# Kernel optimization log

Hardware: AMD Instinct MI355X
Metric: run time of the kernel (lower is better)

Reference implementation:

```python
import jax, jax.numpy as jnp
import numpy as np

B, N, D_IN, D, H, DEPTH = 8, 1024, 256, 256, 8, 3
HD = D // H
EPS = 1e-5


def setup_inputs() -> dict:
    key = jax.random.key(0)
    ks = jax.random.split(key, 16)
    x = jax.random.normal(ks[0], (B, N, D_IN), dtype=jnp.float32)
    # binary adjacency with self-loops (requires_grad=False Parameter in torch)
    adj = (jax.random.uniform(ks[1], (N, N)) < 0.03).astype(jnp.float32)
    adj = jnp.maximum(adj, jnp.eye(N, dtype=jnp.float32))
    s = 1.0 / np.sqrt(D)
    W0 = jax.random.uniform(ks[2], (D, D_IN), minval=-s, maxval=s)
    Wq = jax.random.uniform(ks[3], (DEPTH, D, D), minval=-s, maxval=s)
    Wk = jax.random.uniform(ks[4], (DEPTH, D, D), minval=-s, maxval=s)
    Wv = jax.random.uniform(ks[5], (DEPTH, D, D), minval=-s, maxval=s)
    Wo = jax.random.uniform(ks[6], (DEPTH, D, D), minval=-s, maxval=s)
    bq = jnp.zeros((DEPTH, D)); bk = jnp.zeros((DEPTH, D))
    bv = jnp.zeros((DEPTH, D)); bo = jnp.zeros((DEPTH, D))
    gamma = jnp.ones((DEPTH, D)); beta = jnp.zeros((DEPTH, D))
    return {"x": x, "adj": adj, "W0": W0, "Wq": Wq, "bq": bq, "Wk": Wk,
            "bk": bk, "Wv": Wv, "bv": bv, "Wo": Wo, "bo": bo,
            "gamma": gamma, "beta": beta}


def _layernorm(h, g, b):
    mu = jnp.mean(h, axis=-1, keepdims=True)
    var = jnp.mean(jnp.square(h - mu), axis=-1, keepdims=True)
    return (h - mu) * jax.lax.rsqrt(var + EPS) * g + b


def reference(x, adj, W0, Wq, bq, Wk, bk, Wv, bv, Wo, bo, gamma, beta):
    # input projection (no bias)
    h = jnp.einsum('bnd,ed->bne', x, W0)  # [B,N,D]
    mask = adj[None, None] > 0            # [1,1,N,N]
    scale = 1.0 / jnp.sqrt(jnp.float32(HD))
    atten = None
    for i in range(DEPTH):
        q = (jnp.einsum('bnd,ed->bne', h, Wq[i]) + bq[i]).reshape(B, N, H, HD)
        k = (jnp.einsum('bnd,ed->bne', h, Wk[i]) + bk[i]).reshape(B, N, H, HD)
        v = (jnp.einsum('bnd,ed->bne', h, Wv[i]) + bv[i]).reshape(B, N, H, HD)
        scores = jnp.einsum('bihd,bjhd->bhij', q, k) * scale  # [B,H,N,N]
        scores = jnp.where(mask, scores, -1e9)
        a = jax.nn.softmax(scores, axis=-1)
        o = jnp.einsum('bhij,bjhd->bihd', a, v).reshape(B, N, D)
        y = jnp.einsum('bnd,ed->bne', o, Wo[i]) + bo[i]
        h = _layernorm(h + y, gamma[i], beta[i])
        a_mean = jnp.mean(a, axis=1)  # head-averaged [B,N,N]
        atten = a_mean if atten is None else jnp.einsum('bij,bjk->bik', a_mean, atten)
    return h, atten
```

## Files before the change

### kernel.cpp

```cpp
#include <hip/hip_runtime.h>

typedef unsigned short u16;
typedef unsigned int   u32;
typedef float  f32x4  __attribute__((ext_vector_type(4)));
typedef __bf16 bf16x8 __attribute__((ext_vector_type(8)));
typedef u32    u32x4  __attribute__((ext_vector_type(4)));
typedef u32    u32x2  __attribute__((ext_vector_type(2)));

#define Bb  8
#define Nn  1024
#define Dd  256
#define Hh  8
#define HDd 32
#define CAP 96

__device__ __forceinline__ float bf2f(u16 s){
  u32 u = ((u32)s) << 16; float f; __builtin_memcpy(&f, &u, 4); return f;
}
__device__ __forceinline__ u16 f2bf(float f){
  u32 u; __builtin_memcpy(&u, &f, 4);
  u = (u + 0x7fffu + ((u >> 16) & 1u)) >> 16;
  return (u16)u;
}
__device__ __forceinline__ f32x4 mfma16(bf16x8 a, bf16x8 b, f32x4 c){
  return __builtin_amdgcn_mfma_f32_16x16x32_bf16(a, b, c, 0, 0, 0);
}
__device__ __forceinline__ bf16x8 ld_bf8(const u16* p){
  u32x4 u = *(const u32x4*)p; bf16x8 r; __builtin_memcpy(&r, &u, 16); return r;
}

__global__ void f32_to_bf16(const float* __restrict__ src, u16* __restrict__ dst, int n){
  int i = (blockIdx.x * 256 + threadIdx.x) * 4;
  if (i < n){
    f32x4 v = *(const f32x4*)(src + i);
    u32x2 p;
    p[0] = (u32)f2bf(v[0]) | ((u32)f2bf(v[1]) << 16);
    p[1] = (u32)f2bf(v[2]) | ((u32)f2bf(v[3]) << 16);
    *(u32x2*)(dst + i) = p;
  }
}

__global__ void conv_w4(const float* __restrict__ wq, const float* __restrict__ wk,
                        const float* __restrict__ wv, const float* __restrict__ wo,
                        u16* __restrict__ dst){
  int g = blockIdx.x * 256 + threadIdx.x;
  int sec = g / 49152, off = (g - sec * 49152) * 4;
  const float* src = (sec == 0 ? wq : sec == 1 ? wk : sec == 2 ? wv : wo);
  f32x4 v = *(const f32x4*)(src + off);
  u32x2 p;
  p[0] = (u32)f2bf(v[0]) | ((u32)f2bf(v[1]) << 16);
  p[1] = (u32)f2bf(v[2]) | ((u32)f2bf(v[3]) << 16);
  *(u32x2*)(dst + sec * 196608 + off) = p;
}

__global__ void bias_concat(const float* __restrict__ bq, const float* __restrict__ bk,
                            const float* __restrict__ bv, float* __restrict__ bqkv){
  int t = threadIdx.x;
  for (int l = 0; l < 3; ++l){
    bqkv[l*768 +       t] = bq[l*256 + t];
    bqkv[l*768 + 256 + t] = bk[l*256 + t];
    bqkv[l*768 + 512 + t] = bv[l*256 + t];
  }
}

__global__ void adj_to_bits(const float* __restrict__ adj, u32* __restrict__ bits){
  int w = blockIdx.x * 256 + threadIdx.x;
  const float* p = adj + (long)w * 32;
  u32 m = 0;
  #pragma unroll
  for (int t = 0; t < 32; t += 4){
    f32x4 v = *(const f32x4*)(p + t);
    if (v[0] != 0.f) m |= 1u << (t+0);
    if (v[1] != 0.f) m |= 1u << (t+1);
    if (v[2] != 0.f) m |= 1u << (t+2);
    if (v[3] != 0.f) m |= 1u << (t+3);
  }
  bits[w] = m;
}

__global__ __launch_bounds__(256) void nbr_build(const u32* __restrict__ bits,
                                                 u16* __restrict__ idx, int* __restrict__ cnt){
  int i = blockIdx.x * 256 + threadIdx.x;
  int c = 0;
  for (int w = 0; w < 32; ++w){
    u32 wd = bits[i*32 + w];
    while (wd){
      int bi = __ffs(wd) - 1; wd &= wd - 1;
      if (c < CAP) idx[(long)i*CAP + c] = (u16)(w*32 + bi);
      ++c;
    }
  }
  cnt[i] = (c < CAP) ? c : CAP;
}

template<bool HBC, bool HBR, bool OF, bool OB>
__global__ __launch_bounds__(256,2) void gemm_bt(
    const u16* __restrict__ A, int lda, long sA,
    const u16* __restrict__ Bt, int ldb, long sB,
    float* __restrict__ Cf, u16* __restrict__ Cb, int ldc, long sC,
    int K, const float* __restrict__ bc, long sbc, const float* __restrict__ br)
{
  __shared__ u16 As[128][40];
  __shared__ u16 Bs[128][40];
  const int bz = blockIdx.z;
  const u16* Ap = A + (long)bz * sA;
  const u16* Bp = Bt + (long)bz * sB;
  const long co = (long)bz * sC;
  const int m0 = blockIdx.y * 128, n0 = blockIdx.x * 128;
  const int tid = threadIdx.x, wave = tid >> 6, lane = tid & 63;
  const int arow = lane & 15, agrp = lane >> 4;
  const int wr = (wave >> 1) * 64, wc = (wave & 1) * 64;
  const int srow = tid >> 1, sch = (tid & 1) * 16;
  const u16* ga = Ap + (long)(m0 + srow) * lda + sch;
  const u16* gb = Bp + (long)(n0 + srow) * ldb + sch;
  f32x4 acc[4][4] = {};
  for (int kb = 0; kb < K; kb += 32){
    u32x4 a0 = *(const u32x4*)ga; u32x4 a1 = *(const u32x4*)(ga + 8);
    u32x4 b0 = *(const u32x4*)gb; u32x4 b1 = *(const u32x4*)(gb + 8);
    __syncthreads();
    *(u32x4*)&As[srow][sch] = a0; *(u32x4*)&As[srow][sch + 8] = a1;
    *(u32x4*)&Bs[srow][sch] = b0; *(u32x4*)&Bs[srow][sch + 8] = b1;
    __syncthreads();
    ga += 32; gb += 32;
    bf16x8 af[4], bv[4];
    #pragma unroll
    for (int f = 0; f < 4; ++f){
      af[f] = ld_bf8(&As[wr + f*16 + arow][agrp*8]);
      bv[f] = ld_bf8(&Bs[wc + f*16 + arow][agrp*8]);
    }
    #pragma unroll
    for (int fm = 0; fm < 4; ++fm)
      #pragma unroll
      for (int fn = 0; fn < 4; ++fn)
        acc[fm][fn] = mfma16(af[fm], bv[fn], acc[fm][fn]);
  }
  #pragma unroll
  for (int fm = 0; fm < 4; ++fm){
    #pragma unroll
    for (int fn = 0; fn < 4; ++fn){
      int j = n0 + wc + fn*16 + arow;
      float badd = 0.f;
      if (HBC) badd = bc[(long)bz*sbc + j];
      #pragma unroll
      for (int r = 0; r < 4; ++r){
        int i = m0 + wr + fm*16 + agrp*4 + r;
        float v = acc[fm][fn][r] + badd;
        if (HBR) v += br[i];
        long idx = co + (long)i * ldc + j;
        if (OF) Cf[idx] = v;
        if (OB) Cb[idx] = f2bf(v);
      }
    }
  }
}

__global__ __launch_bounds__(256) void attn_sparse(
    const u16* __restrict__ qkv,
    u16* __restrict__ ob,
    const u16* __restrict__ idxg, const int* __restrict__ cntg,
    float* __restrict__ amv)
{
  __shared__ float qs[4][256];
  __shared__ float E[4][CAP][8];
  __shared__ float invl[4][8];
  __shared__ u16   idxl[4][CAP];
  __shared__ int   cntl[4];
  const int b = blockIdx.y, i0 = blockIdx.x * 4;
  const int tid = threadIdx.x, w = tid >> 6, lane = tid & 63;
  const float SCALE = 0.17677669529663687f;

  { int e = tid * 4, rr = e >> 8, c = e & 255;
    u32x2 uv = *(const u32x2*)(qkv + ((long)(b*Nn + i0 + rr)) * 768 + c);
    qs[rr][c+0] = SCALE * bf2f((u16)(uv[0] & 0xffff));
    qs[rr][c+1] = SCALE * bf2f((u16)(uv[0] >> 16));
    qs[rr][c+2] = SCALE * bf2f((u16)(uv[1] & 0xffff));
    qs[rr][c+3] = SCALE * bf2f((u16)(uv[1] >> 16)); }
  for (int s = tid; s < 4*CAP; s += 256){
    int rr = s / CAP, ss = s - rr*CAP;
    idxl[rr][ss] = idxg[(long)(i0 + rr)*CAP + ss];
  }
  if (tid < 4) cntl[tid] = cntg[i0 + tid];
  __syncthreads();

  const int i = i0 + w;
  const int cnt = cntl[w];

  { const f32x4 qreg = *(const f32x4*)&qs[w][lane*4];
    const int h = lane >> 3;
    int s = 0;
    for (; s + 2 <= cnt; s += 2){
      int ja = idxl[w][s], jb = idxl[w][s+1];
      u32x2 ka = *(const u32x2*)(qkv + ((long)(b*Nn + ja))*768 + 256 + lane*4);
      u32x2 kb = *(const u32x2*)(qkv + ((long)(b*Nn + jb))*768 + 256 + lane*4);
      float pa = qreg[0]*bf2f((u16)(ka[0]&0xffff)) + qreg[1]*bf2f((u16)(ka[0]>>16))
               + qreg[2]*bf2f((u16)(ka[1]&0xffff)) + qreg[3]*bf2f((u16)(ka[1]>>16));
      float pb = qreg[0]*bf2f((u16)(kb[0]&0xffff)) + qreg[1]*bf2f((u16)(kb[0]>>16))
               + qreg[2]*bf2f((u16)(kb[1]&0xffff)) + qreg[3]*bf2f((u16)(kb[1]>>16));
      pa += __shfl_xor(pa, 1, 64); pa += __shfl_xor(pa, 2, 64); pa += __shfl_xor(pa, 4, 64);
      pb += __shfl_xor(pb, 1, 64); pb += __shfl_xor(pb, 2, 64); pb += __shfl_xor(pb, 4, 64);
      if ((lane & 7) == 0){ E[w][s][h] = pa; E[w][s+1][h] = pb; }
    }
    if (s < cnt){
      int ja = idxl[w][s];
      u32x2 ka = *(const u32x2*)(qkv + ((long)(b*Nn + ja))*768 + 256 + lane*4);
      float pa = qreg[0]*bf2f((u16)(ka[0]&0xffff)) + qreg[1]*bf2f((u16)(ka[0]>>16))
               + qreg[2]*bf2f((u16)(ka[1]&0xffff)) + qreg[3]*bf2f((u16)(ka[1]>>16));
      pa += __shfl_xor(pa, 1, 64); pa += __shfl_xor(pa, 2, 64); pa += __shfl_xor(pa, 4, 64);
      if ((lane & 7) == 0) E[w][s][h] = pa;
    }
  }
  __syncthreads();

  { const int h = lane >> 3, k = lane & 7;
    float m = -3.0e38f;
    for (int s = k; s < cnt; s += 8) m = fmaxf(m, E[w][s][h]);
    m = fmaxf(m, __shfl_xor(m, 1, 64));
    m = fmaxf(m, __shfl_xor(m, 2, 64));
    m = fmaxf(m, __shfl_xor(m, 4, 64));
    float l = 0.f;
    for (int s = k; s < cnt; s += 8){
      float e = __expf(E[w][s][h] - m);
      E[w][s][h] = e; l += e;
    }
    l += __shfl_xor(l, 1, 64);
    l += __shfl_xor(l, 2, 64);
    l += __shfl_xor(l, 4, 64);
    if (k == 0) invl[w][h] = 1.f / l;
  }
  __syncthreads();

  { f32x4 i0v = *(f32x4*)&invl[w][0], i1v = *(f32x4*)&invl[w][4];
    for (int s = lane; s < cnt; s += 64){
      f32x4 e0 = *(f32x4*)&E[w][s][0], e1 = *(f32x4*)&E[w][s][4];
      float a = e0[0]*i0v[0] + e0[1]*i0v[1] + e0[2]*i0v[2] + e0[3]*i0v[3]
              + e1[0]*i1v[0] + e1[1]*i1v[1] + e1[2]*i1v[2] + e1[3]*i1v[3];
      amv[((long)(b*Nn + i))*CAP + s] = a * 0.125f;
    }
  }

  { const int d0 = lane * 4, h = lane >> 3;
    f32x4 acc = {0.f, 0.f, 0.f, 0.f};
    int s = 0;
    for (; s + 2 <= cnt; s += 2){
      int ja = idxl[w][s], jb = idxl[w][s+1];
      u32x2 va = *(const u32x2*)(qkv + ((long)(b*Nn + ja)) * 768 + 512 + d0);
      u32x2 vb = *(const u32x2*)(qkv + ((long)(b*Nn + jb)) * 768 + 512 + d0);
      float ea = E[w][s][h], eb = E[w][s+1][h];
      acc[0] += ea * bf2f((u16)(va[0] & 0xffff)) + eb * bf2f((u16)(vb[0] & 0xffff));
      acc[1] += ea * bf2f((u16)(va[0] >> 16))    + eb * bf2f((u16)(vb[0] >> 16));
      acc[2] += ea * bf2f((u16)(va[1] & 0xffff)) + eb * bf2f((u16)(vb[1] & 0xffff));
      acc[3] += ea * bf2f((u16)(va[1] >> 16))    + eb * bf2f((u16)(vb[1] >> 16));
    }
    if (s < cnt){
      int ja = idxl[w][s];
      u32x2 va = *(const u32x2*)(qkv + ((long)(b*Nn + ja)) * 768 + 512 + d0);
      float ea = E[w][s][h];
      acc[0] += ea * bf2f((u16)(va[0] & 0xffff));
      acc[1] += ea * bf2f((u16)(va[0] >> 16));
      acc[2] += ea * bf2f((u16)(va[1] & 0xffff));
      acc[3] += ea * bf2f((u16)(va[1] >> 16));
    }
    float nl = invl[w][h];
    u32x2 pb;
    pb[0] = (u32)f2bf(acc[0]*nl) | ((u32)f2bf(acc[1]*nl) << 16);
    pb[1] = (u32)f2bf(acc[2]*nl) | ((u32)f2bf(acc[3]*nl) << 16);
    *(u32x2*)(ob + ((long)(b*Nn + i)) * 256 + d0) = pb;
  }
}

__global__ __launch_bounds__(256) void sp_gemm1(
    const float* __restrict__ amv1, const float* __restrict__ amv0,
    const u16* __restrict__ idxg, const int* __restrict__ cntg,
    u16* __restrict__ P1)
{
  __shared__ float accum[1024];
  __shared__ u16 idxl[CAP];
  __shared__ u16 cjl[CAP];
  __shared__ float v1[CAP];
  const int b = blockIdx.y, i = blockIdx.x, tid = threadIdx.x;
  { f32x4 z = {0.f,0.f,0.f,0.f}; *(f32x4*)&accum[tid*4] = z; }
  const int cnt = cntg[i];
  if (tid < CAP){
    idxl[tid] = idxg[(long)i*CAP + tid];
    v1[tid]   = amv1[((long)(b*Nn + i))*CAP + tid];
  }
  __syncthreads();
  if (tid < CAP)
    cjl[tid] = (tid < cnt) ? (u16)cntg[idxl[tid]] : (u16)0;
  __syncthreads();
  const int npairs = cnt * 64;
  for (int p = tid; p < npairs; p += 512){
    const int sa = p >> 6, ta = p & 63;
    const int ja = idxl[sa], ca = cjl[sa];
    const float va = v1[sa];
    int colA = 0, colA2 = 0; float prA = 0.f, prA2 = 0.f;
    const bool dA  = ta < ca;
    const bool dA2 = ta + 64 < ca;
    if (dA){  colA  = idxg[(long)ja*CAP + ta];
              prA   = va * amv0[((long)(b*Nn + ja))*CAP + ta]; }
    if (dA2){ colA2 = idxg[(long)ja*CAP + ta + 64];
              prA2  = va * amv0[((long)(b*Nn + ja))*CAP + ta + 64]; }
    const int pb = p + 256;
    const bool hasB = pb < npairs;
    const int sb = pb >> 6, tb = pb & 63;
    int jb = 0, cb = 0; float vb = 0.f;
    if (hasB){ jb = idxl[sb]; cb = cjl[sb]; vb = v1[sb]; }
    int colB = 0, colB2 = 0; float prB = 0.f, prB2 = 0.f;
    const bool dB  = hasB && tb < cb;
    const bool dB2 = hasB && tb + 64 < cb;
    if (dB){  colB  = idxg[(long)jb*CAP + tb];
              prB   = vb * amv0[((long)(b*Nn + jb))*CAP + tb]; }
    if (dB2){ colB2 = idxg[(long)jb*CAP + tb + 64];
              prB2  = vb * amv0[((long)(b*Nn + jb))*CAP + tb + 64]; }
    if (dA)  atomicAdd(&accum[colA],  prA);
    if (dA2) atomicAdd(&accum[colA2], prA2);
    if (dB)  atomicAdd(&accum[colB],  prB);
    if (dB2) atomicAdd(&accum[colB2], prB2);
  }
  __syncthreads();
  int c0 = tid * 4;
  u32x2 pb;
  pb[0] = (u32)f2bf(accum[c0])   | ((u32)f2bf(accum[c0+1]) << 16);
  pb[1] = (u32)f2bf(accum[c0+2]) | ((u32)f2bf(accum[c0+3]) << 16);
  *(u32x2*)(P1 + ((long)(b*Nn + i))*1024 + c0) = pb;
}

__global__ __launch_bounds__(256) void sp_gemm2(
    const float* __restrict__ amv2, const u16* __restrict__ P1,
    const u16* __restrict__ idxg, const int* __restrict__ cntg,
    float* __restrict__ out)
{
  __shared__ u16 idxl[CAP];
  __shared__ float v2[CAP];
  const int b = blockIdx.y, i = blockIdx.x, tid = threadIdx.x;
  const int cnt = cntg[i];
  if (tid < CAP){
    idxl[tid] = idxg[(long)i*CAP + tid];
    v2[tid]   = amv2[((long)(b*Nn + i))*CAP + tid];
  }
  __syncthreads();
  f32x4 acc = {0.f, 0.f, 0.f, 0.f};
  const int c0 = tid * 4;
  int s = 0;
  for (; s + 2 <= cnt; s += 2){
    int ja = idxl[s], jb = idxl[s+1];
    float ea = v2[s], eb = v2[s+1];
    u32x2 va = *(const u32x2*)(P1 + ((long)(b*Nn + ja))*1024 + c0);
    u32x2 vb = *(const u32x2*)(P1 + ((long)(b*Nn + jb))*1024 + c0);
    acc[0] += ea * bf2f((u16)(va[0] & 0xffff)) + eb * bf2f((u16)(vb[0] & 0xffff));
    acc[1] += ea * bf2f((u16)(va[0] >> 16))    + eb * bf2f((u16)(vb[0] >> 16));
    acc[2] += ea * bf2f((u16)(va[1] & 0xffff)) + eb * bf2f((u16)(vb[1] & 0xffff));
    acc[3] += ea * bf2f((u16)(va[1] >> 16))    + eb * bf2f((u16)(vb[1] >> 16));
  }
  if (s < cnt){
    int ja = idxl[s];
    float ea = v2[s];
    u32x2 va = *(const u32x2*)(P1 + ((long)(b*Nn + ja))*1024 + c0);
    acc[0] += ea * bf2f((u16)(va[0] & 0xffff));
    acc[1] += ea * bf2f((u16)(va[0] >> 16));
    acc[2] += ea * bf2f((u16)(va[1] & 0xffff));
    acc[3] += ea * bf2f((u16)(va[1] >> 16));
  }
  *(f32x4*)(out + ((long)(b*Nn + i))*1024 + c0) = acc;
}

__global__ __launch_bounds__(256) void ln_kernel(
    const float* __restrict__ hin, const float* __restrict__ y,
    float* __restrict__ hout, u16* __restrict__ hb, float* __restrict__ outf,
    const float* __restrict__ g, const float* __restrict__ be)
{
  int row  = blockIdx.x * 4 + (threadIdx.x >> 6);
  int lane = threadIdx.x & 63;
  f32x4 v = *(const f32x4*)(hin + (long)row*Dd + lane*4)
          + *(const f32x4*)(y   + (long)row*Dd + lane*4);
  float s = v[0] + v[1] + v[2] + v[3];
  #pragma unroll
  for (int off = 32; off; off >>= 1) s += __shfl_xor(s, off, 64);
  float mu = s * (1.f/256.f);
  f32x4 d = v - mu;
  float q2 = d[0]*d[0] + d[1]*d[1] + d[2]*d[2] + d[3]*d[3];
  #pragma unroll
  for (int off = 32; off; off >>= 1) q2 += __shfl_xor(q2, off, 64);
  float rs = rsqrtf(q2 * (1.f/256.f) + 1e-5f);
  f32x4 ov;
  #pragma unroll
  for (int p = 0; p < 4; ++p)
    ov[p] = d[p] * rs * g[lane*4 + p] + be[lane*4 + p];
  *(f32x4*)(hout + (long)row*Dd + lane*4) = ov;
  if (hb){
    u32x2 pb;
    pb[0] = (u32)f2bf(ov[0]) | ((u32)f2bf(ov[1]) << 16);
    pb[1] = (u32)f2bf(ov[2]) | ((u32)f2bf(ov[3]) << 16);
    *(u32x2*)(hb + (long)row*Dd + lane*4) = pb;
  }
  if (outf)
    *(f32x4*)(outf + (long)row*Dd + lane*4) = ov;
}

extern "C" void kernel_launch(void* const* d_in, const int* in_sizes, int n_in,
                              void* d_out, int out_size, void* d_ws, size_t ws_size,
                              hipStream_t stream)
{
  (void)in_sizes; (void)n_in; (void)out_size; (void)ws_size;
  const float* x   = (const float*)d_in[0];
  const float* adj = (const float*)d_in[1];
  const float* W0  = (const float*)d_in[2];
  const float* Wq  = (const float*)d_in[3];
  const float* bq  = (const float*)d_in[4];
  const float* Wk  = (const float*)d_in[5];
  const float* bk  = (const float*)d_in[6];
  const float* Wv  = (const float*)d_in[7];
  const float* bv  = (const float*)d_in[8];
  const float* Wo  = (const float*)d_in[9];
  const float* bo  = (const float*)d_in[10];
  const float* gm  = (const float*)d_in[11];
  const float* bt  = (const float*)d_in[12];
  float* outf  = (float*)d_out;
  float* outat = outf + (long)Bb * Nn * Dd;

  char* w = (char*)d_ws;
  u16* W0b  = (u16*)w; w += 131072;
  u16* Wqb  = (u16*)w; w += 393216;
  u16* Wkb  = (u16*)w; w += 393216;
  u16* Wvb  = (u16*)w; w += 393216;
  u16* Wob  = (u16*)w; w += 393216;
  float* bqkv = (float*)w; w += 9216;
  u32* bitsg = (u32*)w; w += 131072;
  u16* idxg  = (u16*)w; w += 1024*CAP*2;
  int* cntg  = (int*)w; w += 4096;
  u16* xb  = (u16*)w; w += 4194304;
  u16* hb  = (u16*)w; w += 4194304;
  u16* qkv = (u16*)w; w += (long)Bb*Nn*768*2;
  u16* ob  = (u16*)w; w += 4194304;
  float* hbuf = (float*)w; w += 8388608;
  float* ybuf = (float*)w; w += 8388608;
  float* amv0 = (float*)w; w += (long)Bb*Nn*CAP*4;
  float* amv1 = (float*)w; w += (long)Bb*Nn*CAP*4;
  float* amv2 = (float*)w; w += (long)Bb*Nn*CAP*4;
  u16* P1   = (u16*)w; w += 16777216;
  float* amvl[3] = {amv0, amv1, amv2};

  dim3 blk(256);
  f32_to_bf16<<<2048, blk, 0, stream>>>(x,  xb,  2097152);
  f32_to_bf16<<<64,   blk, 0, stream>>>(W0, W0b, 65536);
  conv_w4<<<768, blk, 0, stream>>>(Wq, Wk, Wv, Wo, Wqb);
  bias_concat<<<1, blk, 0, stream>>>(bq, bk, bv, bqkv);
  adj_to_bits<<<128, blk, 0, stream>>>(adj, bitsg);
  nbr_build<<<4, blk, 0, stream>>>(bitsg, idxg, cntg);

  gemm_bt<false,false,true,true><<<dim3(2,64,1), blk, 0, stream>>>(
      xb, 256, 0, W0b, 256, 0, hbuf, hb, 256, 0, 256, nullptr, 0, nullptr);

  for (int l = 0; l < 3; ++l){
    gemm_bt<true,false,false,true><<<dim3(2,64,3), blk, 0, stream>>>(
        hb, 256, 0, Wqb + (long)l*65536, 256, 196608,
        nullptr, qkv, 768, 256, 256, bqkv + l*768, 256, nullptr);
    attn_sparse<<<dim3(256,8), blk, 0, stream>>>(qkv, ob, idxg, cntg, amvl[l]);
    gemm_bt<true,false,true,false><<<dim3(2,64,1), blk, 0, stream>>>(
        ob, 256, 0, Wob + (long)l*65536, 256, 0, ybuf, nullptr, 256, 0, 256,
        bo + l*256, 0, nullptr);
    ln_kernel<<<dim3(2048), blk, 0, stream>>>(
        hbuf, ybuf, hbuf, (l < 2 ? hb : nullptr), (l < 2 ? nullptr : outf),
        gm + l*256, bt + l*256);
    if (l == 1)
      sp_gemm1<<<dim3(1024,8), blk, 0, stream>>>(amv1, amv0, idxg, cntg, P1);
    if (l == 2)
      sp_gemm2<<<dim3(1024,8), blk, 0, stream>>>(amv2, P1, idxg, cntg, outat);
  }
}
```

Before: 305.7 us.

## Write layer-0 attention densely and reuse row-gather kernel for both attention products

Layer 0 attention weights are now scattered as bf16 into a dense zeroed NxN buffer, so the first attention product becomes a sparse-row gather over dense rows instead of a shared-memory atomic scatter. The two product kernels merge into one templated kernel. Weight and bias conversion kernels are fused into one launch. The trade is a 16 MB memset plus dense bf16 reads, and extra rounding of the layer-0 weights to bf16.

New measurement: 287.1 us. -6.1%, faster.

```diff
diff --git a/kernel.cpp b/kernel.cpp
--- a/kernel.cpp
+++ b/kernel.cpp
@@ -40,27 +40,34 @@
   }
 }
 
-__global__ void conv_w4(const float* __restrict__ wq, const float* __restrict__ wk,
-                        const float* __restrict__ wv, const float* __restrict__ wo,
-                        u16* __restrict__ dst){
-  int g = blockIdx.x * 256 + threadIdx.x;
-  int sec = g / 49152, off = (g - sec * 49152) * 4;
-  const float* src = (sec == 0 ? wq : sec == 1 ? wk : sec == 2 ? wv : wo);
+__global__ void conv_w5(const float* __restrict__ w0, const float* __restrict__ wq,
+                        const float* __restrict__ wk, const float* __restrict__ wv,
+                        const float* __restrict__ wo, u16* __restrict__ dst,
+                        const float* __restrict__ bq, const float* __restrict__ bk,
+                        const float* __restrict__ bv, float* __restrict__ bqkv){
+  if (blockIdx.x == 832){
+    int t = threadIdx.x;
+    for (int l = 0; l < 3; ++l){
+      bqkv[l*768 +       t] = bq[l*256 + t];
+      bqkv[l*768 + 256 + t] = bk[l*256 + t];
+      bqkv[l*768 + 512 + t] = bv[l*256 + t];
+    }
+    return;
+  }
+  int g4 = (blockIdx.x * 256 + threadIdx.x) * 4;
+  const float* src;
+  int off;
+  if (g4 < 65536){ src = w0; off = g4; }
+  else {
+    int g = g4 - 65536;
+    int sec = g / 196608; off = g - sec * 196608;
+    src = (sec == 0 ? wq : sec == 1 ? wk : sec == 2 ? wv : wo);
+  }
   f32x4 v = *(const f32x4*)(src + off);
   u32x2 p;
   p[0] = (u32)f2bf(v[0]) | ((u32)f2bf(v[1]) << 16);
   p[1] = (u32)f2bf(v[2]) | ((u32)f2bf(v[3]) << 16);
-  *(u32x2*)(dst + sec * 196608 + off) = p;
-}
-
-__global__ void bias_concat(const float* __restrict__ bq, const float* __restrict__ bk,
-                            const float* __restrict__ bv, float* __restrict__ bqkv){
-  int t = threadIdx.x;
-  for (int l = 0; l < 3; ++l){
-    bqkv[l*768 +       t] = bq[l*256 + t];
-    bqkv[l*768 + 256 + t] = bk[l*256 + t];
-    bqkv[l*768 + 512 + t] = bv[l*256 + t];
-  }
+  *(u32x2*)(dst + g4) = p;
 }
 
 __global__ void adj_to_bits(const float* __restrict__ adj, u32* __restrict__ bits){
@@ -158,7 +165,8 @@
     const u16* __restrict__ qkv,
     u16* __restrict__ ob,
     const u16* __restrict__ idxg, const int* __restrict__ cntg,
-    float* __restrict__ amv)
+    float* __restrict__ amv,
+    u16* __restrict__ amd, int dense)
 {
   __shared__ float qs[4][256];
   __shared__ float E[4][CAP][8];
@@ -234,7 +242,9 @@
       f32x4 e0 = *(f32x4*)&E[w][s][0], e1 = *(f32x4*)&E[w][s][4];
       float a = e0[0]*i0v[0] + e0[1]*i0v[1] + e0[2]*i0v[2] + e0[3]*i0v[3]
               + e1[0]*i1v[0] + e1[1]*i1v[1] + e1[2]*i1v[2] + e1[3]*i1v[3];
-      amv[((long)(b*Nn + i))*CAP + s] = a * 0.125f;
+      a *= 0.125f;
+      if (dense) amd[((long)(b*Nn + i))*1024 + idxl[w][s]] = f2bf(a);
+      else       amv[((long)(b*Nn + i))*CAP + s] = a;
     }
   }
 
@@ -268,75 +278,20 @@
   }
 }
 
-__global__ __launch_bounds__(256) void sp_gemm1(
-    const float* __restrict__ amv1, const float* __restrict__ amv0,
+template<bool OUTF32>
+__global__ __launch_bounds__(256) void sp_chain(
+    const float* __restrict__ wts,
+    const u16* __restrict__ rows,
     const u16* __restrict__ idxg, const int* __restrict__ cntg,
-    u16* __restrict__ P1)
-{
-  __shared__ float accum[1024];
-  __shared__ u16 idxl[CAP];
-  __shared__ u16 cjl[CAP];
-  __shared__ float v1[CAP];
-  const int b = blockIdx.y, i = blockIdx.x, tid = threadIdx.x;
-  { f32x4 z = {0.f,0.f,0.f,0.f}; *(f32x4*)&accum[tid*4] = z; }
-  const int cnt = cntg[i];
-  if (tid < CAP){
-    idxl[tid] = idxg[(long)i*CAP + tid];
-    v1[tid]   = amv1[((long)(b*Nn + i))*CAP + tid];
-  }
-  __syncthreads();
-  if (tid < CAP)
-    cjl[tid] = (tid < cnt) ? (u16)cntg[idxl[tid]] : (u16)0;
-  __syncthreads();
-  const int npairs = cnt * 64;
-  for (int p = tid; p < npairs; p += 512){
-    const int sa = p >> 6, ta = p & 63;
-    const int ja = idxl[sa], ca = cjl[sa];
-    const float va = v1[sa];
-    int colA = 0, colA2 = 0; float prA = 0.f, prA2 = 0.f;
-    const bool dA  = ta < ca;
-    const bool dA2 = ta + 64 < ca;
-    if (dA){  colA  = idxg[(long)ja*CAP + ta];
-              prA   = va * amv0[((long)(b*Nn + ja))*CAP + ta]; }
-    if (dA2){ colA2 = idxg[(long)ja*CAP + ta + 64];
-              prA2  = va * amv0[((long)(b*Nn + ja))*CAP + ta + 64]; }
-    const int pb = p + 256;
-    const bool hasB = pb < npairs;
-    const int sb = pb >> 6, tb = pb & 63;
-    int jb = 0, cb = 0; float vb = 0.f;
-    if (hasB){ jb = idxl[sb]; cb = cjl[sb]; vb = v1[sb]; }
-    int colB = 0, colB2 = 0; float prB = 0.f, prB2 = 0.f;
-    const bool dB  = hasB && tb < cb;
-    const bool dB2 = hasB && tb + 64 < cb;
-    if (dB){  colB  = idxg[(long)jb*CAP + tb];
-              prB   = vb * amv0[((long)(b*Nn + jb))*CAP + tb]; }
-    if (dB2){ colB2 = idxg[(long)jb*CAP + tb + 64];
-              prB2  = vb * amv0[((long)(b*Nn + jb))*CAP + tb + 64]; }
-    if (dA)  atomicAdd(&accum[colA],  prA);
-    if (dA2) atomicAdd(&accum[colA2], prA2);
-    if (dB)  atomicAdd(&accum[colB],  prB);
-    if (dB2) atomicAdd(&accum[colB2], prB2);
-  }
-  __syncthreads();
-  int c0 = tid * 4;
-  u32x2 pb;
-  pb[0] = (u32)f2bf(accum[c0])   | ((u32)f2bf(accum[c0+1]) << 16);
-  pb[1] = (u32)f2bf(accum[c0+2]) | ((u32)f2bf(accum[c0+3]) << 16);
-  *(u32x2*)(P1 + ((long)(b*Nn + i))*1024 + c0) = pb;
-}
-
-__global__ __launch_bounds__(256) void sp_gemm2(
-    const float* __restrict__ amv2, const u16* __restrict__ P1,
-    const u16* __restrict__ idxg, const int* __restrict__ cntg,
-    float* __restrict__ out)
+    u16* __restrict__ dstb, float* __restrict__ dstf)
 {
   __shared__ u16 idxl[CAP];
-  __shared__ float v2[CAP];
+  __shared__ float wl[CAP];
   const int b = blockIdx.y, i = blockIdx.x, tid = threadIdx.x;
   const int cnt = cntg[i];
   if (tid < CAP){
     idxl[tid] = idxg[(long)i*CAP + tid];
-    v2[tid]   = amv2[((long)(b*Nn + i))*CAP + tid];
+    wl[tid]   = wts[((long)(b*Nn + i))*CAP + tid];
   }
   __syncthreads();
   f32x4 acc = {0.f, 0.f, 0.f, 0.f};
@@ -344,9 +299,9 @@
   int s = 0;
   for (; s + 2 <= cnt; s += 2){
     int ja = idxl[s], jb = idxl[s+1];
-    float ea = v2[s], eb = v2[s+1];
-    u32x2 va = *(const u32x2*)(P1 + ((long)(b*Nn + ja))*1024 + c0);
-    u32x2 vb = *(const u32x2*)(P1 + ((long)(b*Nn + jb))*1024 + c0);
+    float ea = wl[s], eb = wl[s+1];
+    u32x2 va = *(const u32x2*)(rows + ((long)(b*Nn + ja))*1024 + c0);
+    u32x2 vb = *(const u32x2*)(rows + ((long)(b*Nn + jb))*1024 + c0);
     acc[0] += ea * bf2f((u16)(va[0] & 0xffff)) + eb * bf2f((u16)(vb[0] & 0xffff));
     acc[1] += ea * bf2f((u16)(va[0] >> 16))    + eb * bf2f((u16)(vb[0] >> 16));
     acc[2] += ea * bf2f((u16)(va[1] & 0xffff)) + eb * bf2f((u16)(vb[1] & 0xffff));
@@ -354,14 +309,21 @@
   }
   if (s < cnt){
     int ja = idxl[s];
-    float ea = v2[s];
-    u32x2 va = *(const u32x2*)(P1 + ((long)(b*Nn + ja))*1024 + c0);
+    float ea = wl[s];
+    u32x2 va = *(const u32x2*)(rows + ((long)(b*Nn + ja))*1024 + c0);
     acc[0] += ea * bf2f((u16)(va[0] & 0xffff));
     acc[1] += ea * bf2f((u16)(va[0] >> 16));
     acc[2] += ea * bf2f((u16)(va[1] & 0xffff));
     acc[3] += ea * bf2f((u16)(va[1] >> 16));
   }
-  *(f32x4*)(out + ((long)(b*Nn + i))*1024 + c0) = acc;
+  if (OUTF32){
+    *(f32x4*)(dstf + ((long)(b*Nn + i))*1024 + c0) = acc;
+  } else {
+    u32x2 pb;
+    pb[0] = (u32)f2bf(acc[0]) | ((u32)f2bf(acc[1]) << 16);
+    pb[1] = (u32)f2bf(acc[2]) | ((u32)f2bf(acc[3]) << 16);
+    *(u32x2*)(dstb + ((long)(b*Nn + i))*1024 + c0) = pb;
+  }
 }
 
 __global__ __launch_bounds__(256) void ln_kernel(
@@ -420,10 +382,7 @@
 
   char* w = (char*)d_ws;
   u16* W0b  = (u16*)w; w += 131072;
-  u16* Wqb  = (u16*)w; w += 393216;
-  u16* Wkb  = (u16*)w; w += 393216;
-  u16* Wvb  = (u16*)w; w += 393216;
-  u16* Wob  = (u16*)w; w += 393216;
+  u16* Wqb  = (u16*)w; w += 4*393216;
   float* bqkv = (float*)w; w += 9216;
   u32* bitsg = (u32*)w; w += 131072;
   u16* idxg  = (u16*)w; w += 1024*CAP*2;
@@ -434,17 +393,15 @@
   u16* ob  = (u16*)w; w += 4194304;
   float* hbuf = (float*)w; w += 8388608;
   float* ybuf = (float*)w; w += 8388608;
-  float* amv0 = (float*)w; w += (long)Bb*Nn*CAP*4;
   float* amv1 = (float*)w; w += (long)Bb*Nn*CAP*4;
   float* amv2 = (float*)w; w += (long)Bb*Nn*CAP*4;
   u16* P1   = (u16*)w; w += 16777216;
-  float* amvl[3] = {amv0, amv1, amv2};
+  u16* am0d = (u16*)w; w += 16777216;
 
   dim3 blk(256);
-  f32_to_bf16<<<2048, blk, 0, stream>>>(x,  xb,  2097152);
-  f32_to_bf16<<<64,   blk, 0, stream>>>(W0, W0b, 65536);
-  conv_w4<<<768, blk, 0, stream>>>(Wq, Wk, Wv, Wo, Wqb);
-  bias_concat<<<1, blk, 0, stream>>>(bq, bk, bv, bqkv);
+  hipMemsetAsync(am0d, 0, (size_t)16777216, stream);
+  f32_to_bf16<<<2048, blk, 0, stream>>>(x, xb, 2097152);
+  conv_w5<<<833, blk, 0, stream>>>(W0, Wq, Wk, Wv, Wo, W0b, bq, bk, bv, bqkv);
   adj_to_bits<<<128, blk, 0, stream>>>(adj, bitsg);
   nbr_build<<<4, blk, 0, stream>>>(bitsg, idxg, cntg);
 
@@ -455,16 +412,20 @@
     gemm_bt<true,false,false,true><<<dim3(2,64,3), blk, 0, stream>>>(
         hb, 256, 0, Wqb + (long)l*65536, 256, 196608,
         nullptr, qkv, 768, 256, 256, bqkv + l*768, 256, nullptr);
-    attn_sparse<<<dim3(256,8), blk, 0, stream>>>(qkv, ob, idxg, cntg, amvl[l]);
+    attn_sparse<<<dim3(256,8), blk, 0, stream>>>(
+        qkv, ob, idxg, cntg,
+        (l == 1 ? amv1 : amv2), am0d, (l == 0) ? 1 : 0);
     gemm_bt<true,false,true,false><<<dim3(2,64,1), blk, 0, stream>>>(
-        ob, 256, 0, Wob + (long)l*65536, 256, 0, ybuf, nullptr, 256, 0, 256,
+        ob, 256, 0, Wqb + (long)(3*3+l)*65536, 256, 0, ybuf, nullptr, 256, 0, 256,
         bo + l*256, 0, nullptr);
     ln_kernel<<<dim3(2048), blk, 0, stream>>>(
         hbuf, ybuf, hbuf, (l < 2 ? hb : nullptr), (l < 2 ? nullptr : outf),
         gm + l*256, bt + l*256);
     if (l == 1)
-      sp_gemm1<<<dim3(1024,8), blk, 0, stream>>>(amv1, amv0, idxg, cntg, P1);
+      sp_chain<false><<<dim3(1024,8), blk, 0, stream>>>(
+          amv1, am0d, idxg, cntg, P1, nullptr);
     if (l == 2)
-      sp_gemm2<<<dim3(1024,8), blk, 0, stream>>>(amv2, P1, idxg, cntg, outat);
-  }
-}
+      sp_chain<true><<<dim3(1024,8), blk, 0, stream>>>(
+          amv2, P1, idxg, cntg, nullptr, outat);
+  }
+}
```
